# Kernel tuning notes

Hardware: AMD Instinct MI355X
Metric: run time of the kernel (lower is better)

The kernel has to match this reference:

```python
import jax, jax.numpy as jnp
import numpy as np

B, D, H, W, C = 4, 16, 16, 16, 64

def setup_inputs() -> dict:
    key = jax.random.key(0)
    x = jax.random.normal(key, (B, D, H, W, C), dtype=jnp.float32)
    return {"x": x}

def reference(x):
    b, d, h, w, c = x.shape
    n = d * h * w
    t = x.reshape(b, n, c)                      # [B, N, C] tokens
    scores = jnp.einsum('bic,bjc->bij', t, t)   # [B, N, N], Q=K=V, no scaling (matches source)
    attn = jax.nn.softmax(scores, axis=-1)      # softmax over last axis (keras default)
    out = jnp.einsum('bij,bjc->bic', attn, t)   # [B, N, C]
    return out.reshape(b, d, h, w, c)
```

## Files before the change

kernel.cpp:

```cpp
#include <hip/hip_runtime.h>
#include <stdint.h>

#define B_ 4
#define N_ 4096
#define C_ 64
#define LOG2E 1.44269504088896340736f
#define MSTATIC 100.0f
#define TK_ELEMS (B_ * N_ * C_)
#define VIMG_SH 4096
#define OSTR 68

typedef __attribute__((ext_vector_type(8)))  short bf16x8;
typedef __attribute__((ext_vector_type(4)))  float f32x4;
typedef __attribute__((ext_vector_type(16))) float f32x16;

union PUn { uint32_t u[4]; bf16x8 v; };

static __device__ __forceinline__ short f2bf(float f) {
    union { float f; uint32_t u; } v; v.f = f;
    uint32_t u = v.u;
    return (short)((u + 0x7fffu + ((u >> 16) & 1u)) >> 16);
}

static __device__ __forceinline__ uint32_t pkbf(float a, float b) {
    uint32_t r;
    asm("v_cvt_pk_bf16_f32 %0, %1, %2" : "=v"(r) : "v"(a), "v"(b));
    return r;
}

static __device__ __forceinline__ float xhalf_add(float x) { return x + __shfl_xor(x, 32); }

#define EXP2(x) __builtin_amdgcn_exp2f(x)

__global__ __launch_bounds__(256) void prepass(const float* __restrict__ x,
                                               short* __restrict__ tk,
                                               short* __restrict__ tvT) {
    int gid = blockIdx.x * 256 + threadIdx.x;
    int f = gid * 8;
    f32x4 a  = *(const f32x4*)(x + f);
    f32x4 b4 = *(const f32x4*)(x + f + 4);
    short s[8];
    #pragma unroll
    for (int i = 0; i < 4; ++i) { s[i] = f2bf(a[i]); s[4 + i] = f2bf(b4[i]); }
    bf16x8 pk;
    #pragma unroll
    for (int i = 0; i < 8; ++i) pk[i] = s[i];
    *(bf16x8*)(tk + f) = pk;

    int c0  = f & 63;
    int row = f >> 6;
    int jg  = row & (N_ - 1);
    int bb  = row >> 12;
    int tile = jg >> 6, j = jg & 63;
    int pos = (j & ~12) | ((j & 4) << 1) | ((j & 8) >> 1);
    short* tb = tvT + (size_t)(bb * 64 + tile) * VIMG_SH;
    int base = (pos >> 3) * 512 + (pos & 7);
    #pragma unroll
    for (int i = 0; i < 8; ++i) tb[base + (c0 + i) * 8] = s[i];
}

static __device__ __forceinline__ void kload(bf16x8 kf[4][2], const short* tkb,
                                             int t, int lq, int h) {
    const short* r0 = tkb + ((size_t)(t * 64 + lq)) * C_ + 8 * h;
    #pragma unroll
    for (int s = 0; s < 4; ++s) {
        kf[s][0] = *(const bf16x8*)(r0 + 16 * s);
        kf[s][1] = *(const bf16x8*)(r0 + 32 * C_ + 16 * s);
    }
}

static __device__ __forceinline__ void vload(bf16x8 vf[8], const short* tvb,
                                             int t, int lq, int h) {
    const short* vb = tvb + (size_t)t * VIMG_SH + h * 512 + lq * 8;
    vf[0] = *(const bf16x8*)(vb);
    vf[1] = *(const bf16x8*)(vb + 256);
    vf[2] = *(const bf16x8*)(vb + 1024);
    vf[3] = *(const bf16x8*)(vb + 1280);
    vf[4] = *(const bf16x8*)(vb + 2048);
    vf[5] = *(const bf16x8*)(vb + 2304);
    vf[6] = *(const bf16x8*)(vb + 3072);
    vf[7] = *(const bf16x8*)(vb + 3328);
}

#define MFMA32(A, Bv, Cv) __builtin_amdgcn_mfma_f32_32x32x16_bf16((A), (Bv), (Cv), 0, 0, 0)

#define BODY(DO_PRE) do {                                                          \
    bf16x8 vf[8];                                                                  \
    vload(vf, tvb, tcur, lq, h);                                                   \
    __builtin_amdgcn_s_setprio(1);                                                 \
    f32x16 s0_ = MFMA32(kf[0][0], bq0[0], minit16);                                \
    f32x16 s1_ = MFMA32(kf[0][1], bq0[0], minit16);                                \
    f32x16 s2_ = MFMA32(kf[0][0], bq1[0], minit16);                                \
    f32x16 s3_ = MFMA32(kf[0][1], bq1[0], minit16);                                \
    s0_ = MFMA32(kf[1][0], bq0[1], s0_);  s1_ = MFMA32(kf[1][1], bq0[1], s1_);     \
    s2_ = MFMA32(kf[1][0], bq1[1], s2_);  s3_ = MFMA32(kf[1][1], bq1[1], s3_);     \
    s0_ = MFMA32(kf[2][0], bq0[2], s0_);  s1_ = MFMA32(kf[2][1], bq0[2], s1_);     \
    s2_ = MFMA32(kf[2][0], bq1[2], s2_);  s3_ = MFMA32(kf[2][1], bq1[2], s3_);     \
    s0_ = MFMA32(kf[3][0], bq0[3], s0_);  s1_ = MFMA32(kf[3][1], bq0[3], s1_);     \
    s2_ = MFMA32(kf[3][0], bq1[3], s2_);  s3_ = MFMA32(kf[3][1], bq1[3], s3_);     \
    __builtin_amdgcn_s_setprio(0);                                                 \
    if (DO_PRE) kload(kf, tkb, tcur + 1, lq, h);                                   \
    float rsA_ = 0.f, rsB_ = 0.f, rsC_ = 0.f, rsD_ = 0.f;                          \
    float rsE_ = 0.f, rsF_ = 0.f, rsG_ = 0.f, rsH_ = 0.f;                          \
    PUn pf0_, pf1_, pf2_, pf3_, pf4_, pf5_, pf6_, pf7_;                            \
    _Pragma("unroll")                                                              \
    for (int k_ = 0; k_ < 4; ++k_) {                                               \
        { float e0_ = EXP2(s0_[2*k_]),   e1_ = EXP2(s0_[2*k_+1]);                  \
          pf0_.u[k_] = pkbf(e0_, e1_); rsA_ += e0_ + e1_; }                        \
        { float e0_ = EXP2(s0_[8+2*k_]), e1_ = EXP2(s0_[9+2*k_]);                  \
          pf1_.u[k_] = pkbf(e0_, e1_); rsB_ += e0_ + e1_; }                        \
        { float e0_ = EXP2(s1_[2*k_]),   e1_ = EXP2(s1_[2*k_+1]);                  \
          pf2_.u[k_] = pkbf(e0_, e1_); rsC_ += e0_ + e1_; }                        \
        { float e0_ = EXP2(s1_[8+2*k_]), e1_ = EXP2(s1_[9+2*k_]);                  \
          pf3_.u[k_] = pkbf(e0_, e1_); rsD_ += e0_ + e1_; }                        \
        { float e0_ = EXP2(s2_[2*k_]),   e1_ = EXP2(s2_[2*k_+1]);                  \
          pf4_.u[k_] = pkbf(e0_, e1_); rsE_ += e0_ + e1_; }                        \
        { float e0_ = EXP2(s2_[8+2*k_]), e1_ = EXP2(s2_[9+2*k_]);                  \
          pf5_.u[k_] = pkbf(e0_, e1_); rsF_ += e0_ + e1_; }                        \
        { float e0_ = EXP2(s3_[2*k_]),   e1_ = EXP2(s3_[2*k_+1]);                  \
          pf6_.u[k_] = pkbf(e0_, e1_); rsG_ += e0_ + e1_; }                        \
        { float e0_ = EXP2(s3_[8+2*k_]), e1_ = EXP2(s3_[9+2*k_]);                  \
          pf7_.u[k_] = pkbf(e0_, e1_); rsH_ += e0_ + e1_; }                        \
    }                                                                              \
    l0 += (rsA_ + rsB_) + (rsC_ + rsD_);                                           \
    l1 += (rsE_ + rsF_) + (rsG_ + rsH_);                                           \
    __builtin_amdgcn_s_setprio(1);                                                 \
    o00 = MFMA32(vf[0], pf0_.v, o00);  o01 = MFMA32(vf[1], pf0_.v, o01);           \
    o10 = MFMA32(vf[0], pf4_.v, o10);  o11 = MFMA32(vf[1], pf4_.v, o11);           \
    o00 = MFMA32(vf[2], pf1_.v, o00);  o01 = MFMA32(vf[3], pf1_.v, o01);           \
    o10 = MFMA32(vf[2], pf5_.v, o10);  o11 = MFMA32(vf[3], pf5_.v, o11);           \
    o00 = MFMA32(vf[4], pf2_.v, o00);  o01 = MFMA32(vf[5], pf2_.v, o01);           \
    o10 = MFMA32(vf[4], pf6_.v, o10);  o11 = MFMA32(vf[5], pf6_.v, o11);           \
    o00 = MFMA32(vf[6], pf3_.v, o00);  o01 = MFMA32(vf[7], pf3_.v, o01);           \
    o10 = MFMA32(vf[6], pf7_.v, o10);  o11 = MFMA32(vf[7], pf7_.v, o11);           \
    __builtin_amdgcn_s_setprio(0);                                                 \
    ++tcur;                                                                        \
} while (0)

__global__ __launch_bounds__(256, 1) void denoiser_attn(const float* __restrict__ x,
                                                        const short* __restrict__ tk,
                                                        const short* __restrict__ tvT,
                                                        float* __restrict__ out) {
    __shared__ __align__(16) float epi[4][64 * OSTR];
    __shared__ float lbuf[4][64];

    const int tid  = threadIdx.x;
    const int w    = tid >> 6;
    const int lane = tid & 63;
    const int lq   = lane & 31;
    const int h    = lane >> 5;

    const int swz = ((blockIdx.x & 7) << 5) | (blockIdx.x >> 3);
    const int b   = swz >> 6;
    const int q0  = (swz & 63) << 6;

    const short* tkb = tk + (size_t)(b * N_) * C_;
    const short* tvb = tvT + (size_t)(b * 64) * VIMG_SH;

    int tcur = 16 * w;

    bf16x8 kf[4][2];
    kload(kf, tkb, tcur, lq, h);

    bf16x8 bq0[4], bq1[4];
    {
        const float* qr0 = x + ((size_t)(b * N_ + q0 + lq)) * C_ + 8 * h;
        const float* qr1 = qr0 + 32 * C_;
        #pragma unroll
        for (int s = 0; s < 4; ++s) {
            f32x4 a0 = *(const f32x4*)(qr0 + 16 * s);
            f32x4 b0 = *(const f32x4*)(qr0 + 16 * s + 4);
            f32x4 a1 = *(const f32x4*)(qr1 + 16 * s);
            f32x4 b1 = *(const f32x4*)(qr1 + 16 * s + 4);
            bf16x8 q8, q9;
            #pragma unroll
            for (int i = 0; i < 4; ++i) {
                q8[i]     = f2bf(a0[i] * LOG2E);
                q8[4 + i] = f2bf(b0[i] * LOG2E);
                q9[i]     = f2bf(a1[i] * LOG2E);
                q9[4 + i] = f2bf(b1[i] * LOG2E);
            }
            bq0[s] = q8;
            bq1[s] = q9;
        }
    }

    f32x16 minit16;
    #pragma unroll
    for (int i = 0; i < 16; ++i) minit16[i] = -MSTATIC;
    f32x16 o00, o01, o10, o11;
    #pragma unroll
    for (int i = 0; i < 16; ++i) { o00[i] = 0.f; o01[i] = 0.f; o10[i] = 0.f; o11[i] = 0.f; }
    float l0 = 0.f, l1 = 0.f;

    #pragma unroll 1
    for (int tt = 0; tt < 15; ++tt) BODY(1);
    BODY(0);

    l0 = xhalf_add(l0);
    l1 = xhalf_add(l1);

    {
        float* ow = epi[w];
        #pragma unroll
        for (int rg = 0; rg < 4; ++rg) {
            f32x4 a0, a1, b0, b1;
            #pragma unroll
            for (int i = 0; i < 4; ++i) {
                a0[i] = o00[4 * rg + i]; a1[i] = o01[4 * rg + i];
                b0[i] = o10[4 * rg + i]; b1[i] = o11[4 * rg + i];
            }
            const int cb = 8 * rg + 4 * h;
            *(f32x4*)&ow[lq * OSTR + cb]             = a0;
            *(f32x4*)&ow[lq * OSTR + cb + 32]        = a1;
            *(f32x4*)&ow[(32 + lq) * OSTR + cb]      = b0;
            *(f32x4*)&ow[(32 + lq) * OSTR + cb + 32] = b1;
        }
        if (h == 0) { lbuf[w][lq] = l0; lbuf[w][32 + lq] = l1; }
    }
    __syncthreads();

    {
        const int q  = tid >> 2;
        const int c0 = (tid & 3) << 4;
        float L = lbuf[0][q] + lbuf[1][q] + lbuf[2][q] + lbuf[3][q];
        const float inv = 1.f / L;
        f32x4 acc0 = (f32x4){0.f,0.f,0.f,0.f}, acc1 = acc0, acc2 = acc0, acc3 = acc0;
        #pragma unroll
        for (int u = 0; u < 4; ++u) {
            const float* pu = epi[u] + q * OSTR + c0;
            f32x4 v0 = *(const f32x4*)(pu);
            f32x4 v1 = *(const f32x4*)(pu + 4);
            f32x4 v2 = *(const f32x4*)(pu + 8);
            f32x4 v3 = *(const f32x4*)(pu + 12);
            #pragma unroll
            for (int i = 0; i < 4; ++i) {
                acc0[i] += v0[i]; acc1[i] += v1[i];
                acc2[i] += v2[i]; acc3[i] += v3[i];
            }
        }
        #pragma unroll
        for (int i = 0; i < 4; ++i) {
            acc0[i] *= inv; acc1[i] *= inv; acc2[i] *= inv; acc3[i] *= inv;
        }
        float* op = out + ((size_t)(b * N_ + q0 + q)) * C_ + c0;
        *(f32x4*)(op)      = acc0;
        *(f32x4*)(op + 4)  = acc1;
        *(f32x4*)(op + 8)  = acc2;
        *(f32x4*)(op + 12) = acc3;
    }
}

extern "C" void kernel_launch(void* const* d_in, const int* in_sizes, int n_in,
                              void* d_out, int out_size, void* d_ws, size_t ws_size,
                              hipStream_t stream) {
    (void)in_sizes; (void)n_in; (void)out_size; (void)ws_size;
    const float* x = (const float*)d_in[0];
    float* out = (float*)d_out;
    short* tk  = (short*)d_ws;
    short* tvT = tk + TK_ELEMS;

    hipLaunchKernelGGL(prepass, dim3(TK_ELEMS / 8 / 256), dim3(256), 0, stream, x, tk, tvT);
    hipLaunchKernelGGL(denoiser_attn, dim3(256), dim3(256), 0, stream, x, tk, tvT, out);
}
```

Before: 35.47 us.

## Split key range across two blocks with partial outputs and combine kernel

Splits each query tile's key range in half across two blocks (512 blocks instead of 256), so more workgroups are available to fill the device's compute units. Each block writes unnormalized partial outputs and row sums to workspace, and a new combine kernel sums the two halves and normalizes. The inner body is also restructured into two sequential 32-row sub-passes per key tile, lowering live score registers. This costs an extra kernel launch, extra global traffic for the partial planes, and a larger workspace.

```diff
diff --git a/kernel.cpp b/kernel.cpp
--- a/kernel.cpp
+++ b/kernel.cpp
@@ -9,6 +9,8 @@
 #define TK_ELEMS (B_ * N_ * C_)
 #define VIMG_SH 4096
 #define OSTR 68
+#define PO_PLANE (B_ * N_ * C_)
+#define PL_PLANE (B_ * N_)
 
 typedef __attribute__((ext_vector_type(8)))  short bf16x8;
 typedef __attribute__((ext_vector_type(4)))  float f32x4;
@@ -84,25 +86,16 @@
 
 #define MFMA32(A, Bv, Cv) __builtin_amdgcn_mfma_f32_32x32x16_bf16((A), (Bv), (Cv), 0, 0, 0)
 
-#define BODY(DO_PRE) do {                                                          \
-    bf16x8 vf[8];                                                                  \
-    vload(vf, tvb, tcur, lq, h);                                                   \
+#define SUBBODY(BQ, OA, OB, LACC) do {                                             \
     __builtin_amdgcn_s_setprio(1);                                                 \
-    f32x16 s0_ = MFMA32(kf[0][0], bq0[0], minit16);                                \
-    f32x16 s1_ = MFMA32(kf[0][1], bq0[0], minit16);                                \
-    f32x16 s2_ = MFMA32(kf[0][0], bq1[0], minit16);                                \
-    f32x16 s3_ = MFMA32(kf[0][1], bq1[0], minit16);                                \
-    s0_ = MFMA32(kf[1][0], bq0[1], s0_);  s1_ = MFMA32(kf[1][1], bq0[1], s1_);     \
-    s2_ = MFMA32(kf[1][0], bq1[1], s2_);  s3_ = MFMA32(kf[1][1], bq1[1], s3_);     \
-    s0_ = MFMA32(kf[2][0], bq0[2], s0_);  s1_ = MFMA32(kf[2][1], bq0[2], s1_);     \
-    s2_ = MFMA32(kf[2][0], bq1[2], s2_);  s3_ = MFMA32(kf[2][1], bq1[2], s3_);     \
-    s0_ = MFMA32(kf[3][0], bq0[3], s0_);  s1_ = MFMA32(kf[3][1], bq0[3], s1_);     \
-    s2_ = MFMA32(kf[3][0], bq1[3], s2_);  s3_ = MFMA32(kf[3][1], bq1[3], s3_);     \
+    f32x16 s0_ = MFMA32(kf[0][0], BQ[0], minit16);                                 \
+    f32x16 s1_ = MFMA32(kf[0][1], BQ[0], minit16);                                 \
+    s0_ = MFMA32(kf[1][0], BQ[1], s0_);  s1_ = MFMA32(kf[1][1], BQ[1], s1_);       \
+    s0_ = MFMA32(kf[2][0], BQ[2], s0_);  s1_ = MFMA32(kf[2][1], BQ[2], s1_);       \
+    s0_ = MFMA32(kf[3][0], BQ[3], s0_);  s1_ = MFMA32(kf[3][1], BQ[3], s1_);       \
     __builtin_amdgcn_s_setprio(0);                                                 \
-    if (DO_PRE) kload(kf, tkb, tcur + 1, lq, h);                                   \
     float rsA_ = 0.f, rsB_ = 0.f, rsC_ = 0.f, rsD_ = 0.f;                          \
-    float rsE_ = 0.f, rsF_ = 0.f, rsG_ = 0.f, rsH_ = 0.f;                          \
-    PUn pf0_, pf1_, pf2_, pf3_, pf4_, pf5_, pf6_, pf7_;                            \
+    PUn pf0_, pf1_, pf2_, pf3_;                                                    \
     _Pragma("unroll")                                                              \
     for (int k_ = 0; k_ < 4; ++k_) {                                               \
         { float e0_ = EXP2(s0_[2*k_]),   e1_ = EXP2(s0_[2*k_+1]);                  \
@@ -113,34 +106,21 @@
           pf2_.u[k_] = pkbf(e0_, e1_); rsC_ += e0_ + e1_; }                        \
         { float e0_ = EXP2(s1_[8+2*k_]), e1_ = EXP2(s1_[9+2*k_]);                  \
           pf3_.u[k_] = pkbf(e0_, e1_); rsD_ += e0_ + e1_; }                        \
-        { float e0_ = EXP2(s2_[2*k_]),   e1_ = EXP2(s2_[2*k_+1]);                  \
-          pf4_.u[k_] = pkbf(e0_, e1_); rsE_ += e0_ + e1_; }                        \
-        { float e0_ = EXP2(s2_[8+2*k_]), e1_ = EXP2(s2_[9+2*k_]);                  \
-          pf5_.u[k_] = pkbf(e0_, e1_); rsF_ += e0_ + e1_; }                        \
-        { float e0_ = EXP2(s3_[2*k_]),   e1_ = EXP2(s3_[2*k_+1]);                  \
-          pf6_.u[k_] = pkbf(e0_, e1_); rsG_ += e0_ + e1_; }                        \
-        { float e0_ = EXP2(s3_[8+2*k_]), e1_ = EXP2(s3_[9+2*k_]);                  \
-          pf7_.u[k_] = pkbf(e0_, e1_); rsH_ += e0_ + e1_; }                        \
     }                                                                              \
-    l0 += (rsA_ + rsB_) + (rsC_ + rsD_);                                           \
-    l1 += (rsE_ + rsF_) + (rsG_ + rsH_);                                           \
+    LACC += (rsA_ + rsB_) + (rsC_ + rsD_);                                         \
     __builtin_amdgcn_s_setprio(1);                                                 \
-    o00 = MFMA32(vf[0], pf0_.v, o00);  o01 = MFMA32(vf[1], pf0_.v, o01);           \
-    o10 = MFMA32(vf[0], pf4_.v, o10);  o11 = MFMA32(vf[1], pf4_.v, o11);           \
-    o00 = MFMA32(vf[2], pf1_.v, o00);  o01 = MFMA32(vf[3], pf1_.v, o01);           \
-    o10 = MFMA32(vf[2], pf5_.v, o10);  o11 = MFMA32(vf[3], pf5_.v, o11);           \
-    o00 = MFMA32(vf[4], pf2_.v, o00);  o01 = MFMA32(vf[5], pf2_.v, o01);           \
-    o10 = MFMA32(vf[4], pf6_.v, o10);  o11 = MFMA32(vf[5], pf6_.v, o11);           \
-    o00 = MFMA32(vf[6], pf3_.v, o00);  o01 = MFMA32(vf[7], pf3_.v, o01);           \
-    o10 = MFMA32(vf[6], pf7_.v, o10);  o11 = MFMA32(vf[7], pf7_.v, o11);           \
+    OA = MFMA32(vf[0], pf0_.v, OA);  OB = MFMA32(vf[1], pf0_.v, OB);               \
+    OA = MFMA32(vf[2], pf1_.v, OA);  OB = MFMA32(vf[3], pf1_.v, OB);               \
+    OA = MFMA32(vf[4], pf2_.v, OA);  OB = MFMA32(vf[5], pf2_.v, OB);               \
+    OA = MFMA32(vf[6], pf3_.v, OA);  OB = MFMA32(vf[7], pf3_.v, OB);               \
     __builtin_amdgcn_s_setprio(0);                                                 \
-    ++tcur;                                                                        \
 } while (0)
 
-__global__ __launch_bounds__(256, 1) void denoiser_attn(const float* __restrict__ x,
-                                                        const short* __restrict__ tk,
-                                                        const short* __restrict__ tvT,
-                                                        float* __restrict__ out) {
+__global__ __launch_bounds__(256, 1) void denoiser_attn_part(const float* __restrict__ x,
+                                                             const short* __restrict__ tk,
+                                                             const short* __restrict__ tvT,
+                                                             float* __restrict__ po,
+                                                             float* __restrict__ pl) {
     __shared__ __align__(16) float epi[4][64 * OSTR];
     __shared__ float lbuf[4][64];
 
@@ -150,14 +130,16 @@
     const int lq   = lane & 31;
     const int h    = lane >> 5;
 
-    const int swz = ((blockIdx.x & 7) << 5) | (blockIdx.x >> 3);
-    const int b   = swz >> 6;
-    const int q0  = (swz & 63) << 6;
+    const int swz   = ((blockIdx.x & 7) << 6) | (blockIdx.x >> 3);
+    const int b     = swz >> 7;
+    const int r     = swz & 127;
+    const int q0    = (r >> 1) << 6;
+    const int halfk = r & 1;
 
     const short* tkb = tk + (size_t)(b * N_) * C_;
     const short* tvb = tvT + (size_t)(b * 64) * VIMG_SH;
 
-    int tcur = 16 * w;
+    int tcur = halfk * 32 + 8 * w;
 
     bf16x8 kf[4][2];
     kload(kf, tkb, tcur, lq, h);
@@ -194,8 +176,42 @@
     float l0 = 0.f, l1 = 0.f;
 
     #pragma unroll 1
-    for (int tt = 0; tt < 15; ++tt) BODY(1);
-    BODY(0);
+    for (int tt = 0; tt < 8; ++tt) {
+        bf16x8 vf[8];
+        vload(vf, tvb, tcur, lq, h);
+        SUBBODY(bq0, o00, o01, l0);
+        {
+            __builtin_amdgcn_s_setprio(1);
+            f32x16 s0_ = MFMA32(kf[0][0], bq1[0], minit16);
+            f32x16 s1_ = MFMA32(kf[0][1], bq1[0], minit16);
+            s0_ = MFMA32(kf[1][0], bq1[1], s0_);  s1_ = MFMA32(kf[1][1], bq1[1], s1_);
+            s0_ = MFMA32(kf[2][0], bq1[2], s0_);  s1_ = MFMA32(kf[2][1], bq1[2], s1_);
+            s0_ = MFMA32(kf[3][0], bq1[3], s0_);  s1_ = MFMA32(kf[3][1], bq1[3], s1_);
+            __builtin_amdgcn_s_setprio(0);
+            if (tt < 7) kload(kf, tkb, tcur + 1, lq, h);
+            float rsA_ = 0.f, rsB_ = 0.f, rsC_ = 0.f, rsD_ = 0.f;
+            PUn pf0_, pf1_, pf2_, pf3_;
+            #pragma unroll
+            for (int k_ = 0; k_ < 4; ++k_) {
+                { float e0_ = EXP2(s0_[2*k_]),   e1_ = EXP2(s0_[2*k_+1]);
+                  pf0_.u[k_] = pkbf(e0_, e1_); rsA_ += e0_ + e1_; }
+                { float e0_ = EXP2(s0_[8+2*k_]), e1_ = EXP2(s0_[9+2*k_]);
+                  pf1_.u[k_] = pkbf(e0_, e1_); rsB_ += e0_ + e1_; }
+                { float e0_ = EXP2(s1_[2*k_]),   e1_ = EXP2(s1_[2*k_+1]);
+                  pf2_.u[k_] = pkbf(e0_, e1_); rsC_ += e0_ + e1_; }
+                { float e0_ = EXP2(s1_[8+2*k_]), e1_ = EXP2(s1_[9+2*k_]);
+                  pf3_.u[k_] = pkbf(e0_, e1_); rsD_ += e0_ + e1_; }
+            }
+            l1 += (rsA_ + rsB_) + (rsC_ + rsD_);
+            __builtin_amdgcn_s_setprio(1);
+            o10 = MFMA32(vf[0], pf0_.v, o10);  o11 = MFMA32(vf[1], pf0_.v, o11);
+            o10 = MFMA32(vf[2], pf1_.v, o10);  o11 = MFMA32(vf[3], pf1_.v, o11);
+            o10 = MFMA32(vf[4], pf2_.v, o10);  o11 = MFMA32(vf[5], pf2_.v, o11);
+            o10 = MFMA32(vf[6], pf3_.v, o10);  o11 = MFMA32(vf[7], pf3_.v, o11);
+            __builtin_amdgcn_s_setprio(0);
+        }
+        ++tcur;
+    }
 
     l0 = xhalf_add(l0);
     l1 = xhalf_add(l1);
@@ -224,7 +240,6 @@
         const int q  = tid >> 2;
         const int c0 = (tid & 3) << 4;
         float L = lbuf[0][q] + lbuf[1][q] + lbuf[2][q] + lbuf[3][q];
-        const float inv = 1.f / L;
         f32x4 acc0 = (f32x4){0.f,0.f,0.f,0.f}, acc1 = acc0, acc2 = acc0, acc3 = acc0;
         #pragma unroll
         for (int u = 0; u < 4; ++u) {
@@ -239,16 +254,35 @@
                 acc2[i] += v2[i]; acc3[i] += v3[i];
             }
         }
-        #pragma unroll
-        for (int i = 0; i < 4; ++i) {
-            acc0[i] *= inv; acc1[i] *= inv; acc2[i] *= inv; acc3[i] *= inv;
-        }
-        float* op = out + ((size_t)(b * N_ + q0 + q)) * C_ + c0;
+        float* op = po + (size_t)halfk * PO_PLANE + ((size_t)(b * N_ + q0 + q)) * C_ + c0;
         *(f32x4*)(op)      = acc0;
         *(f32x4*)(op + 4)  = acc1;
         *(f32x4*)(op + 8)  = acc2;
         *(f32x4*)(op + 12) = acc3;
-    }
+        if (c0 == 0) pl[(size_t)halfk * PL_PLANE + b * N_ + q0 + q] = L;
+    }
+}
+
+__global__ __launch_bounds__(256) void combine(const float* __restrict__ po,
+                                               const float* __restrict__ pl,
+                                               float* __restrict__ out) {
+    int gid = blockIdx.x * 256 + threadIdx.x;
+    int base = gid * 8;
+    int row = base >> 6;
+    float L = pl[row] + pl[PL_PLANE + row];
+    float inv = 1.f / L;
+    f32x4 a0 = *(const f32x4*)(po + base);
+    f32x4 a1 = *(const f32x4*)(po + base + 4);
+    f32x4 b0 = *(const f32x4*)(po + PO_PLANE + base);
+    f32x4 b1 = *(const f32x4*)(po + PO_PLANE + base + 4);
+    f32x4 r0, r1;
+    #pragma unroll
+    for (int i = 0; i < 4; ++i) {
+        r0[i] = (a0[i] + b0[i]) * inv;
+        r1[i] = (a1[i] + b1[i]) * inv;
+    }
+    *(f32x4*)(out + base)     = r0;
+    *(f32x4*)(out + base + 4) = r1;
 }
 
 extern "C" void kernel_launch(void* const* d_in, const int* in_sizes, int n_in,
@@ -259,7 +293,10 @@
     float* out = (float*)d_out;
     short* tk  = (short*)d_ws;
     short* tvT = tk + TK_ELEMS;
+    float* po  = (float*)(tvT + TK_ELEMS);
+    float* pl  = po + 2 * (size_t)PO_PLANE;
 
     hipLaunchKernelGGL(prepass, dim3(TK_ELEMS / 8 / 256), dim3(256), 0, stream, x, tk, tvT);
-    hipLaunchKernelGGL(denoiser_attn, dim3(256), dim3(256), 0, stream, x, tk, tvT, out);
-}
+    hipLaunchKernelGGL(denoiser_attn_part, dim3(512), dim3(256), 0, stream, x, tk, tvT, po, pl);
+    hipLaunchKernelGGL(combine, dim3(PO_PLANE / 8 / 256), dim3(256), 0, stream, po, pl, out);
+}
```

New measurement: 45.69 us. 1.29x slower.
